# Optimization experiments

Measured on AMD Instinct MI355X. Metric: run time of the kernel, lower is better.

## Reference

```python
import jax, jax.numpy as jnp
import numpy as np

D_MODEL = 768
N_LAYER = 8
EXPAND = 2
D_INNER = EXPAND * D_MODEL          # 1536
HEADDIM = 64
NHEADS = D_INNER // HEADDIM         # 24
D_STATE = 128
D_CONV = 4
NGROUPS = 1
CONV_DIM = D_INNER + 2 * NGROUPS * D_STATE      # 1792
D_IN_PROJ = 2 * D_INNER + 2 * NGROUPS * D_STATE + NHEADS  # 3352
DIM_INP = 6
DIM_OUT = 5
BATCH = 4
SEQ = 2048
EPS = 1e-5


def rmsnorm(x, w):
    return x * jax.lax.rsqrt(jnp.mean(x * x, axis=-1, keepdims=True) + EPS) * w


def setup_inputs() -> dict:
    key = jax.random.key(0)
    ks = jax.random.split(key, 12)
    nrm = lambda k, shape, s=0.02: jax.random.normal(k, shape, jnp.float32) * s
    x = jax.random.normal(ks[0], (BATCH, SEQ, DIM_INP), jnp.float32)
    y = jax.random.normal(ks[1], (BATCH, SEQ, DIM_OUT), jnp.float32)
    W_emb = nrm(ks[2], (D_MODEL, DIM_INP))
    b_emb = jnp.zeros((D_MODEL,), jnp.float32)
    # stacked per-layer Mamba2 params
    W_in = nrm(ks[3], (N_LAYER, D_IN_PROJ, D_MODEL))
    conv_w = nrm(ks[4], (N_LAYER, CONV_DIM, D_CONV), 0.2)
    conv_b = jnp.zeros((N_LAYER, CONV_DIM), jnp.float32)
    dt0 = jax.random.uniform(ks[5], (N_LAYER, NHEADS), jnp.float32, 1e-3, 1e-1)
    dt_bias = jnp.log(jnp.expm1(dt0))  # inverse softplus of target dt
    A_log = jnp.log(jax.random.uniform(ks[6], (N_LAYER, NHEADS), jnp.float32, 1.0, 16.0))
    Dp = jnp.ones((N_LAYER, NHEADS), jnp.float32)
    norm_w = jnp.ones((N_LAYER, D_INNER), jnp.float32)     # gated RMSNorm inside Mamba2
    W_out = nrm(ks[7], (N_LAYER, D_MODEL, D_INNER))
    block_norm_w = jnp.ones((N_LAYER, D_MODEL), jnp.float32)  # prenorm RMSNorm per block
    norm_f_w = jnp.ones((D_MODEL,), jnp.float32)
    W_head = nrm(ks[8], (DIM_OUT, D_MODEL))
    return dict(x=x, y=y, W_emb=W_emb, b_emb=b_emb, W_in=W_in, conv_w=conv_w,
                conv_b=conv_b, dt_bias=dt_bias, A_log=A_log, Dp=Dp, norm_w=norm_w,
                W_out=W_out, block_norm_w=block_norm_w, norm_f_w=norm_f_w, W_head=W_head)


def _mamba2(u, W_in_l, conv_w_l, conv_b_l, dt_bias_l, A_log_l, D_l, norm_w_l, W_out_l):
    B, L, _ = u.shape
    zxbcdt = jnp.einsum('bld,ed->ble', u, W_in_l)  # [B,L,D_IN_PROJ]
    z = zxbcdt[..., :D_INNER]
    xBC = zxbcdt[..., D_INNER:D_INNER + CONV_DIM]
    dt = jax.nn.softplus(zxbcdt[..., D_INNER + CONV_DIM:] + dt_bias_l)  # [B,L,H]
    # causal depthwise conv1d, kernel D_CONV
    xp = jnp.pad(xBC, ((0, 0), (D_CONV - 1, 0), (0, 0)))
    xBC = sum(xp[:, k:k + L, :] * conv_w_l[:, k] for k in range(D_CONV)) + conv_b_l
    xBC = jax.nn.silu(xBC)
    xh = xBC[..., :D_INNER].reshape(B, L, NHEADS, HEADDIM)
    Bm = xBC[..., D_INNER:D_INNER + D_STATE]   # [B,L,N] (ngroups=1)
    Cm = xBC[..., D_INNER + D_STATE:]          # [B,L,N]
    A = -jnp.exp(A_log_l)                       # [H]
    decay = jnp.exp(dt * A)                     # [B,L,H]
    dtx = dt[..., None] * xh                    # [B,L,H,P]

    def step(h, inp):
        dec_t, dtx_t, B_t, C_t = inp            # [B,H],[B,H,P],[B,N],[B,N]
        h = h * dec_t[..., None, None] + dtx_t[..., None] * B_t[:, None, None, :]
        y_t = jnp.einsum('bhpn,bn->bhp', h, C_t)
        return h, y_t

    h0 = jnp.zeros((B, NHEADS, HEADDIM, D_STATE), u.dtype)
    _, ys = jax.lax.scan(step, h0, (decay.transpose(1, 0, 2), dtx.transpose(1, 0, 2, 3),
                                    Bm.transpose(1, 0, 2), Cm.transpose(1, 0, 2)))
    ys = ys.transpose(1, 0, 2, 3) + xh * D_l[None, None, :, None]  # skip term D*x
    yf = ys.reshape(B, L, D_INNER)
    yf = rmsnorm(yf * jax.nn.silu(z), norm_w_l)  # gated RMSNorm (norm_before_gate=False)
    return jnp.einsum('bld,ed->ble', yf, W_out_l)


def _forward(x, W_emb, b_emb, W_in, conv_w, conv_b, dt_bias, A_log, Dp, norm_w,
             W_out, block_norm_w, norm_f_w, W_head):
    h = jnp.einsum('bli,di->bld', x, W_emb) + b_emb
    res = jnp.zeros_like(h)

    def layer_step(carry, lp):
        h, res = carry
        Wi, cw, cb, dtb, Al, Dl, nw, Wo, bnw = lp
        res = h + res
        hn = rmsnorm(res, bnw)
        h = _mamba2(hn, Wi, cw, cb, dtb, Al, Dl, nw, Wo)
        return (h, res), None

    (h, res), _ = jax.lax.scan(layer_step, (h, res),
                               (W_in, conv_w, conv_b, dt_bias, A_log, Dp, norm_w, W_out, block_norm_w))
    res = h + res
    hn = rmsnorm(res, norm_f_w)
    return jnp.einsum('bld,od->blo', hn, W_head)


def reference(x, y, W_emb, b_emb, W_in, conv_w, conv_b, dt_bias, A_log, Dp, norm_w,
              W_out, block_norm_w, norm_f_w, W_head):
    out = _forward(x, W_emb, b_emb, W_in, conv_w, conv_b, dt_bias, A_log, Dp, norm_w,
                   W_out, block_norm_w, norm_f_w, W_head)
    loss = jnp.mean((out - y) ** 2)
    return out, loss
```

## Files before the change

### kernel.cpp

```cpp
#include <hip/hip_runtime.h>
#include <hip/hip_bf16.h>
#include <math.h>

#define BATCH 4
#define SEQ 2048
#define DMODEL 768
#define NLAYER 8
#define DINNER 1536
#define HEADDIM 64
#define NHEADS 24
#define DSTATE 128
#define CONVDIM 1792
#define DINPROJ 3352
#define NPAD 3456
#define ROWS (BATCH*SEQ)
#define EPS 1e-5f
#define QCH 128
#define NCH (SEQ/QCH)

typedef __bf16 bf16;
typedef bf16 bf16x8 __attribute__((ext_vector_type(8)));
typedef bf16 bf16x4 __attribute__((ext_vector_type(4)));
typedef float f32x4 __attribute__((ext_vector_type(4)));

#define GLD(src, dst) __builtin_amdgcn_global_load_lds( \
    (const __attribute__((address_space(1))) void*)(src), \
    (__attribute__((address_space(3))) void*)(dst), 16, 0, 0)

__device__ __forceinline__ void bar_sync() {
    asm volatile("" ::: "memory");
    __builtin_amdgcn_s_barrier();
    asm volatile("" ::: "memory");
}

__device__ __forceinline__ float fsilu(float x) { return x / (1.f + __expf(-x)); }

__global__ void k_embed(const float* __restrict__ x, const float* __restrict__ We,
                        const float* __restrict__ be, float* __restrict__ res) {
    int idx = blockIdx.x * 256 + threadIdx.x;
    int d = idx % DMODEL; int bl = idx / DMODEL;
    float acc = be[d];
#pragma unroll
    for (int i = 0; i < 6; ++i) acc += x[bl * 6 + i] * We[d * 6 + i];
    res[idx] = acc;
}

__global__ __launch_bounds__(256) void k_rmsnorm(const float* __restrict__ res,
                                                 const float* __restrict__ w,
                                                 bf16* __restrict__ out) {
    __shared__ float sm[4];
    int r = blockIdx.x, tid = threadIdx.x;
    float v[3]; float ss = 0.f;
#pragma unroll
    for (int k = 0; k < 3; ++k) {
        int d = tid + k * 256;
        float t = res[r * DMODEL + d];
        v[k] = t; ss += t * t;
    }
#pragma unroll
    for (int off = 32; off; off >>= 1) ss += __shfl_down(ss, off, 64);
    if ((tid & 63) == 0) sm[tid >> 6] = ss;
    __syncthreads();
    float tot = sm[0] + sm[1] + sm[2] + sm[3];
    float sc = rsqrtf(tot / (float)DMODEL + EPS);
#pragma unroll
    for (int k = 0; k < 3; ++k) {
        int d = tid + k * 256;
        out[r * DMODEL + d] = (bf16)(v[k] * sc * w[d]);
    }
}

__global__ void k_cvt_in(const float* __restrict__ src, bf16* __restrict__ dst) {
    int idx = blockIdx.x * 256 + threadIdx.x;
    int l = idx / (NPAD * DMODEL);
    int rem = idx % (NPAD * DMODEL);
    int n = rem / DMODEL;
    int d = rem % DMODEL;
    dst[idx] = (n < DINPROJ) ? (bf16)src[(long)l * DINPROJ * DMODEL + n * DMODEL + d] : (bf16)0.f;
}
__global__ void k_cvt_out(const float* __restrict__ src, bf16* __restrict__ dst) {
    int idx = blockIdx.x * 256 + threadIdx.x;
    dst[idx] = (bf16)src[idx];
}

template <typename OT, int BM, int BN, bool ACC>
__global__ __launch_bounds__(256) void k_gemm(const bf16* __restrict__ A, const bf16* __restrict__ B,
                                              OT* __restrict__ C, int K, int ldc) {
    constexpr int nWn = BN / 64;
    constexpr int nWm = 4 / nWn;
    constexpr int WMR = BM / nWm;
    constexpr int MI  = WMR / 16;
    constexpr int NI  = 4;
    constexpr int RG  = BM / 4;
    constexpr int BG  = BN / RG;
    __shared__ bf16 As[2][BM * 64];
    __shared__ bf16 Bs[2][BN * 64];
    const int tid = threadIdx.x;
    const int lane = tid & 63;
    const int w = tid >> 6;
    const int wm = w / nWn, wn = w % nWn;
    int wg = blockIdx.x + blockIdx.y * gridDim.x;
    int cpx = (gridDim.x * gridDim.y) >> 3;
    int swz = (wg & 7) * cpx + (wg >> 3);
    int bx = swz % gridDim.x;
    int by = swz / gridDim.x;
    const long rowA0 = (long)bx * BM;
    const long rowB0 = (long)by * BN;
    const int srow = tid >> 3;
    const int scol = ((tid & 7) ^ (srow & 7)) * 8;
    const bf16* Ab = A + rowA0 * K + scol;
    const bf16* Bb = B + rowB0 * K + scol;

    f32x4 acc[MI][NI];
    const f32x4 vz = {0.f, 0.f, 0.f, 0.f};
#pragma unroll
    for (int mi = 0; mi < MI; ++mi)
#pragma unroll
        for (int ni = 0; ni < NI; ++ni) acc[mi][ni] = vz;

    auto stage = [&](int buf, int kt) {
#pragma unroll
        for (int j = 0; j < 4; ++j)
            GLD(Ab + (long)(j * RG + srow) * K + kt, &As[buf][(j * RG + w * 8) * 64]);
#pragma unroll
        for (int j = 0; j < BG; ++j)
            GLD(Bb + (long)(j * RG + srow) * K + kt, &Bs[buf][(j * RG + w * 8) * 64]);
    };
    auto waitv = [&]() {
        if constexpr (BG == 4) asm volatile("s_waitcnt vmcnt(8)" ::: "memory");
        else                   asm volatile("s_waitcnt vmcnt(6)" ::: "memory");
    };
    auto compute = [&](int buf) {
        const char* AsB = (const char*)As[buf];
        const char* BsB = (const char*)Bs[buf];
#pragma unroll
        for (int s = 0; s < 2; ++s) {
            bf16x8 af[MI], bfr[NI];
#pragma unroll
            for (int mi = 0; mi < MI; ++mi) {
                int r = wm * WMR + mi * 16 + (lane & 15);
                af[mi] = *(const bf16x8*)(AsB + r * 128 + ((s * 64 + (lane >> 4) * 16) ^ ((r & 7) << 4)));
            }
#pragma unroll
            for (int ni = 0; ni < NI; ++ni) {
                int r = wn * 64 + ni * 16 + (lane & 15);
                bfr[ni] = *(const bf16x8*)(BsB + r * 128 + ((s * 64 + (lane >> 4) * 16) ^ ((r & 7) << 4)));
            }
#pragma unroll
            for (int mi = 0; mi < MI; ++mi)
#pragma unroll
                for (int ni = 0; ni < NI; ++ni)
                    acc[mi][ni] = __builtin_amdgcn_mfma_f32_16x16x32_bf16(af[mi], bfr[ni], acc[mi][ni], 0, 0, 0);
        }
    };

    stage(0, 0);
    stage(1, 64);
    int cur = 0;
    for (int kt = 128; kt < K; kt += 64) {
        waitv();
        bar_sync();
        compute(cur);
        bar_sync();
        stage(cur, kt);
        cur ^= 1;
    }
    waitv();
    bar_sync();
    compute(cur);
    asm volatile("s_waitcnt vmcnt(0)" ::: "memory");
    bar_sync();
    compute(cur ^ 1);

    const int crow = (lane >> 4) * 4;
    const int ccol = lane & 15;
#pragma unroll
    for (int mi = 0; mi < MI; ++mi)
#pragma unroll
        for (int ni = 0; ni < NI; ++ni) {
            long r0 = rowA0 + wm * WMR + mi * 16 + crow;
            long c0 = rowB0 + wn * 64 + ni * 16 + ccol;
#pragma unroll
            for (int j = 0; j < 4; ++j) {
                if constexpr (ACC) C[(r0 + j) * ldc + c0] += (OT)acc[mi][ni][j];
                else               C[(r0 + j) * ldc + c0]  = (OT)acc[mi][ni][j];
            }
        }
}

__global__ void k_convBC(const bf16* __restrict__ zx, const float* __restrict__ cw,
                         const float* __restrict__ cb, bf16* __restrict__ bc) {
    int idx = blockIdx.x * 256 + threadIdx.x;
    int c8 = idx & 31; int blt = idx >> 5;
    int t = blt % SEQ;
    int ch = DINNER + c8 * 8;
    long bbase = (long)(blt - t) * NPAD;
    float cwa[8][4];
#pragma unroll
    for (int j = 0; j < 8; ++j) {
        float4 tv = *(const float4*)(cw + (ch + j) * 4);
        cwa[j][0] = tv.x; cwa[j][1] = tv.y; cwa[j][2] = tv.z; cwa[j][3] = tv.w;
    }
    float acc[8];
#pragma unroll
    for (int j = 0; j < 8; ++j) acc[j] = cb[ch + j];
#pragma unroll
    for (int k = 0; k < 4; ++k) {
        int tt = t + k - 3;
        if (tt >= 0) {
            bf16x8 v = *(const bf16x8*)(zx + bbase + (long)tt * NPAD + DINNER + ch);
#pragma unroll
            for (int j = 0; j < 8; ++j) acc[j] += (float)v[j] * cwa[j][k];
        }
    }
    bf16x8 o;
#pragma unroll
    for (int j = 0; j < 8; ++j) o[j] = (bf16)fsilu(acc[j]);
    *(bf16x8*)(bc + (long)blt * 256 + c8 * 8) = o;
}

__global__ __launch_bounds__(256) void k_prepL(const bf16* __restrict__ zx, const bf16* __restrict__ bc,
                                               const float* __restrict__ cw_l, const float* __restrict__ cb_l,
                                               const float* __restrict__ dt_bias_l,
                                               const float* __restrict__ Alog,
                                               float* __restrict__ Sarr, float* __restrict__ dtc,
                                               float* __restrict__ Pcb,
                                               bf16* __restrict__ XT, bf16* __restrict__ Lbuf) {
    __shared__ float S_lds[128], wl_lds[128], wtot[2];
    __shared__ bf16 Xs[136 * 64];
    __shared__ bf16 Xw[64 * 128];
    __shared__ bf16 Bt[128 * 128];
    int blk = blockIdx.x;
    int b = blk / (NHEADS * NCH);
    int r = blk % (NHEADS * NCH);
    int h = r / NCH;
    int c = r % NCH;
    int tid = threadIdx.x, lane = tid & 63, wid = tid >> 6;
    long brow0 = (long)b * SEQ + c * QCH;
#pragma unroll
    for (int i = 0; i < 5; ++i) {
        int base = i * 256 + wid * 64;
        if (base < 1048) {
            int idx = base + lane;
            long g = brow0 - 3 + (idx >> 3);
            if (g < 0) g = 0;
            if (g > (long)ROWS - 1) g = (long)ROWS - 1;
            GLD(zx + g * NPAD + DINNER + h * HEADDIM + (idx & 7) * 8,
                (char*)Xs + (long)base * 16);
        }
    }
    float ps = 0.f, dtv = 0.f;
    if (tid < 128) {
        float raw = (float)zx[(brow0 + tid) * NPAD + DINNER + CONVDIM + h] + dt_bias_l[h];
        dtv = (raw > 15.f) ? raw : log1pf(__expf(raw));
        float Ah = -__expf(Alog[h]);
        ps = dtv * Ah;
#pragma unroll
        for (int off = 1; off < 64; off <<= 1) {
            float o = __shfl_up(ps, off, 64);
            if ((tid & 63) >= off) ps += o;
        }
        if ((tid & 63) == 63) wtot[tid >> 6] = ps;
    }
    __syncthreads();
    if (tid < 128) {
        if (tid >= 64) ps += wtot[0];
        S_lds[tid] = ps;
    }
    __syncthreads();
    float Sl = S_lds[127];
    if (tid < 128) {
        wl_lds[tid] = __expf(Sl - ps) * dtv;
        Sarr[blk * QCH + tid] = ps;
        dtc[blk * QCH + tid] = dtv;
        if (tid == 127) Pcb[blk] = __expf(Sl);
    }
    __syncthreads();
    {
        int p = tid >> 2, q = tid & 3;
        float4 cwv = *(const float4*)(cw_l + (h * HEADDIM + p) * 4);
        float cbv = cb_l[h * HEADDIM + p];
        float cwa[4] = {cwv.x, cwv.y, cwv.z, cwv.w};
        char* xtb = (char*)XT + (((long)blk) << 14);
#pragma unroll
        for (int ub = 0; ub < 4; ++ub) {
            int u0 = q * 32 + ub * 8;
            bf16x8 vx, vw;
#pragma unroll
            for (int k = 0; k < 8; ++k) {
                int u = u0 + k;
                float a = cbv;
#pragma unroll
                for (int tt = 0; tt < 4; ++tt) {
                    if (c > 0 || u + tt >= 3)
                        a += (float)Xs[(u + tt) * 64 + p] * cwa[tt];
                }
                bf16 xb = (bf16)fsilu(a);
                vx[k] = xb;
                vw[k] = (bf16)((float)xb * wl_lds[u]);
            }
            long off = (long)((p * 256 + u0 * 2) ^ ((p & 7) << 4));
            *(bf16x8*)(xtb + off) = vx;
            *(bf16x8*)((char*)Xw + off) = vw;
        }
    }
#pragma unroll
    for (int nb = 0; nb < 2; ++nb) {
        __syncthreads();
#pragma unroll
        for (int i = 0; i < 4; ++i) {
            int idx = i * 256 + tid;
            GLD(bc + (brow0 + (idx >> 3)) * 256 + nb * 64 + (idx & 7) * 8,
                (char*)Xs + (i * 256 + wid * 64) * 16);
        }
        __syncthreads();
        int nl = tid >> 2, q = tid & 3;
        int n = nb * 64 + nl;
#pragma unroll
        for (int ub = 0; ub < 4; ++ub) {
            int u0 = q * 32 + ub * 8;
            bf16x8 v;
#pragma unroll
            for (int k = 0; k < 8; ++k) v[k] = Xs[(u0 + k) * 64 + nl];
            long off = (long)((n * 256 + u0 * 2) ^ ((n & 7) << 4));
            *(bf16x8*)((char*)Bt + off) = v;
        }
    }
    __syncthreads();
    f32x4 acc[4][2];
    const f32x4 vz = {0.f, 0.f, 0.f, 0.f};
#pragma unroll
    for (int mi = 0; mi < 4; ++mi)
#pragma unroll
        for (int ni = 0; ni < 2; ++ni) acc[mi][ni] = vz;
    const char* XwB = (const char*)Xw;
    const char* BtB = (const char*)Bt;
    __builtin_amdgcn_s_setprio(1);
#pragma unroll
    for (int ks = 0; ks < 4; ++ks) {
        bf16x8 af[4], bfr[2];
#pragma unroll
        for (int mi = 0; mi < 4; ++mi) {
            int pp = mi * 16 + (lane & 15);
            af[mi] = *(const bf16x8*)(XwB + ((pp * 256 + ks * 64 + (lane >> 4) * 16) ^ ((pp & 7) << 4)));
        }
#pragma unroll
        for (int ni = 0; ni < 2; ++ni) {
            int n = wid * 32 + ni * 16 + (lane & 15);
            bfr[ni] = *(const bf16x8*)(BtB + ((n * 256 + ks * 64 + (lane >> 4) * 16) ^ ((n & 7) << 4)));
        }
#pragma unroll
        for (int mi = 0; mi < 4; ++mi)
#pragma unroll
            for (int ni = 0; ni < 2; ++ni)
                acc[mi][ni] = __builtin_amdgcn_mfma_f32_16x16x32_bf16(af[mi], bfr[ni], acc[mi][ni], 0, 0, 0);
    }
    __builtin_amdgcn_s_setprio(0);
    char* lb = (char*)Lbuf + (((long)blk) << 14);
#pragma unroll
    for (int mi = 0; mi < 4; ++mi)
#pragma unroll
        for (int ni = 0; ni < 2; ++ni)
#pragma unroll
            for (int j = 0; j < 4; ++j) {
                int pp = mi * 16 + (lane >> 4) * 4 + j;
                int n = wid * 32 + ni * 16 + (lane & 15);
                *(bf16*)(lb + ((pp * 256 + n * 2) ^ ((pp & 7) << 4))) = (bf16)acc[mi][ni][j];
            }
}

__global__ __launch_bounds__(256) void k_scanB(bf16* __restrict__ Lbuf, const float* __restrict__ Pc) {
    int bh = blockIdx.x >> 2;
    int q = blockIdx.x & 3;
    int off = (q * 256 + threadIdx.x) * 8;
    long base = ((long)bh * NCH) << 13;
    float s[8] = {0.f};
#pragma unroll
    for (int c = 0; c < NCH; ++c) {
        bf16* p = Lbuf + base + ((long)c << 13) + off;
        bf16x8 L = *(bf16x8*)p;
        bf16x8 I;
#pragma unroll
        for (int k = 0; k < 8; ++k) I[k] = (bf16)s[k];
        float P = Pc[bh * NCH + c];
#pragma unroll
        for (int k = 0; k < 8; ++k) s[k] = P * s[k] + (float)L[k];
        *(bf16x8*)p = I;
    }
}

__global__ __launch_bounds__(512) void k_chunkY(const bf16* __restrict__ bc,
                                                const float* __restrict__ Sarr, const float* __restrict__ dtc,
                                                const float* __restrict__ Dp,
                                                const bf16* __restrict__ XT, const bf16* __restrict__ Lbuf,
                                                bf16* __restrict__ ysb) {
    __shared__ bf16 Cs[128 * 128];
    __shared__ bf16 Bs[128 * 128];
    __shared__ bf16 Xts[64 * 128];
    __shared__ bf16 Is[64 * 128];
    __shared__ float S_lds[128], dt_lds[128];
    int blk = blockIdx.x;
    int b = blk / (NHEADS * NCH);
    int r = blk % (NHEADS * NCH);
    int h = r / NCH;
    int c = r % NCH;
    int tid = threadIdx.x, lane = tid & 63, wid = tid >> 6;
    long brow0 = (long)b * SEQ + c * QCH;
    const char* bcB = (const char*)bc;
#pragma unroll
    for (int i = 0; i < 4; ++i) {
        int trow = i * 32 + wid * 4 + (lane >> 4);
        int blk16 = lane & 15;
        const char* rp = bcB + (brow0 + trow) * 512;
        int sb = (blk16 ^ (trow & 7)) << 4;
        GLD(rp + 256 + sb, (char*)Cs + (i * 32 + wid * 4) * 256);
        GLD(rp + sb,       (char*)Bs + (i * 32 + wid * 4) * 256);
    }
    const char* xt = (const char*)XT + (((long)blk) << 14);
    const char* ib = (const char*)Lbuf + (((long)blk) << 14);
#pragma unroll
    for (int i = 0; i < 2; ++i) {
        GLD(xt + (long)(i * 512 + tid) * 16, (char*)Xts + (i * 512 + wid * 64) * 16);
        GLD(ib + (long)(i * 512 + tid) * 16, (char*)Is + (i * 512 + wid * 64) * 16);
    }
    if (tid < 128) { S_lds[tid] = Sarr[blk * QCH + tid]; dt_lds[tid] = dtc[blk * QCH + tid]; }
    float Dh = Dp[h];
    asm volatile("s_waitcnt vmcnt(4) lgkmcnt(0)" ::: "memory");
    bar_sync();
    const char* CsB = (const char*)Cs;
    char* BsB = (char*)Bs;
    const char* IsB = (const char*)Is;
    const char* XtB = (const char*)Xts;
    const f32x4 vz = {0.f, 0.f, 0.f, 0.f};
    int wmG = wid >> 2, wnG = wid & 3;
    f32x4 accg[4][2];
#pragma unroll
    for (int mi = 0; mi < 4; ++mi)
#pragma unroll
        for (int ni = 0; ni < 2; ++ni) accg[mi][ni] = vz;
#pragma unroll
    for (int ks = 0; ks < 4; ++ks) {
        bf16x8 af[4], bfr[2];
#pragma unroll
        for (int mi = 0; mi < 4; ++mi) {
            int t = wmG * 64 + mi * 16 + (lane & 15);
            af[mi] = *(const bf16x8*)(CsB + ((t * 256 + ks * 64 + (lane >> 4) * 16) ^ ((t & 7) << 4)));
        }
#pragma unroll
        for (int ni = 0; ni < 2; ++ni) {
            int u = wnG * 32 + ni * 16 + (lane & 15);
            bfr[ni] = *(const bf16x8*)(BsB + ((u * 256 + ks * 64 + (lane >> 4) * 16) ^ ((u & 7) << 4)));
        }
#pragma unroll
        for (int mi = 0; mi < 4; ++mi)
#pragma unroll
            for (int ni = 0; ni < 2; ++ni)
                accg[mi][ni] = __builtin_amdgcn_mfma_f32_16x16x32_bf16(af[mi], bfr[ni], accg[mi][ni], 0, 0, 0);
    }
    bar_sync();
#pragma unroll
    for (int mi = 0; mi < 4; ++mi) {
#pragma unroll
        for (int j = 0; j < 4; ++j) {
            int t = wmG * 64 + mi * 16 + (lane >> 4) * 4 + j;
            float St = S_lds[t];
#pragma unroll
            for (int ni = 0; ni < 2; ++ni) {
                int u = wnG * 32 + ni * 16 + (lane & 15);
                float v = 0.f;
                if (u <= t) v = accg[mi][ni][j] * __expf(St - S_lds[u]) * dt_lds[u];
                *(bf16*)(BsB + ((t * 256 + u * 2) ^ ((t & 7) << 4))) = (bf16)v;
            }
        }
    }
    asm volatile("s_waitcnt vmcnt(0) lgkmcnt(0)" ::: "memory");
    bar_sync();
    int wmY = wid >> 1, wnY = wid & 1;
    f32x4 accy[2][2];
#pragma unroll
    for (int mi = 0; mi < 2; ++mi)
#pragma unroll
        for (int ni = 0; ni < 2; ++ni) accy[mi][ni] = vz;
#pragma unroll
    for (int ks = 0; ks < 4; ++ks) {
        bf16x8 af[2], bfr[2];
#pragma unroll
        for (int mi = 0; mi < 2; ++mi) {
            int t = wmY * 32 + mi * 16 + (lane & 15);
            af[mi] = *(const bf16x8*)(CsB + ((t * 256 + ks * 64 + (lane >> 4) * 16) ^ ((t & 7) << 4)));
        }
#pragma unroll
        for (int ni = 0; ni < 2; ++ni) {
            int pp = wnY * 32 + ni * 16 + (lane & 15);
            bfr[ni] = *(const bf16x8*)(IsB + ((pp * 256 + ks * 64 + (lane >> 4) * 16) ^ ((pp & 7) << 4)));
        }
#pragma unroll
        for (int mi = 0; mi < 2; ++mi)
#pragma unroll
            for (int ni = 0; ni < 2; ++ni)
                accy[mi][ni] = __builtin_amdgcn_mfma_f32_16x16x32_bf16(af[mi], bfr[ni], accy[mi][ni], 0, 0, 0);
    }
#pragma unroll
    for (int mi = 0; mi < 2; ++mi)
#pragma unroll
        for (int j = 0; j < 4; ++j) {
            int t = wmY * 32 + mi * 16 + (lane >> 4) * 4 + j;
            float e = __expf(S_lds[t]);
#pragma unroll
            for (int ni = 0; ni < 2; ++ni) accy[mi][ni][j] *= e;
        }
#pragma unroll
    for (int ks = 0; ks < 4; ++ks) {
        bf16x8 af[2], bfr[2];
#pragma unroll
        for (int mi = 0; mi < 2; ++mi) {
            int t = wmY * 32 + mi * 16 + (lane & 15);
            af[mi] = *(const bf16x8*)(BsB + ((t * 256 + ks * 64 + (lane >> 4) * 16) ^ ((t & 7) << 4)));
        }
#pragma unroll
        for (int ni = 0; ni < 2; ++ni) {
            int pp = wnY * 32 + ni * 16 + (lane & 15);
            bfr[ni] = *(const bf16x8*)(XtB + ((pp * 256 + ks * 64 + (lane >> 4) * 16) ^ ((pp & 7) << 4)));
        }
#pragma unroll
        for (int mi = 0; mi < 2; ++mi)
#pragma unroll
            for (int ni = 0; ni < 2; ++ni)
                accy[mi][ni] = __builtin_amdgcn_mfma_f32_16x16x32_bf16(af[mi], bfr[ni], accy[mi][ni], 0, 0, 0);
    }
#pragma unroll
    for (int mi = 0; mi < 2; ++mi)
#pragma unroll
        for (int ni = 0; ni < 2; ++ni)
#pragma unroll
            for (int j = 0; j < 4; ++j) {
                int t = wmY * 32 + mi * 16 + (lane >> 4) * 4 + j;
                int pp = wnY * 32 + ni * 16 + (lane & 15);
                float xv = (float)*(const bf16*)(XtB + ((pp * 256 + t * 2) ^ ((pp & 7) << 4)));
                ysb[(brow0 + t) * DINNER + h * HEADDIM + pp] = (bf16)(accy[mi][ni][j] + Dh * xv);
            }
}

__global__ __launch_bounds__(256) void k_gated(const bf16* __restrict__ ys, const bf16* __restrict__ zx,
                                               const float* __restrict__ w, bf16* __restrict__ out) {
    __shared__ float sm[4];
    int r = blockIdx.x, tid = threadIdx.x;
    float v[6]; float ss = 0.f;
#pragma unroll
    for (int k = 0; k < 6; ++k) {
        int d = tid + k * 256;
        float z = (float)zx[(long)r * NPAD + d];
        float t = (float)ys[(long)r * DINNER + d] * fsilu(z);
        v[k] = t; ss += t * t;
    }
#pragma unroll
    for (int off = 32; off; off >>= 1) ss += __shfl_down(ss, off, 64);
    if ((tid & 63) == 0) sm[tid >> 6] = ss;
    __syncthreads();
    float tot = sm[0] + sm[1] + sm[2] + sm[3];
    float sc = rsqrtf(tot / (float)DINNER + EPS);
#pragma unroll
    for (int k = 0; k < 6; ++k) {
        int d = tid + k * 256;
        out[(long)r * DINNER + d] = (bf16)(v[k] * sc * w[d]);
    }
}

__global__ __launch_bounds__(256) void k_head(const bf16* __restrict__ hn, const float* __restrict__ Wh,
                                              const float* __restrict__ y, float* __restrict__ out,
                                              float* __restrict__ loss) {
    __shared__ float sl[4];
    int tid = threadIdx.x, lane = tid & 63, wid = tid >> 6;
    float wv[5][12];
#pragma unroll
    for (int o = 0; o < 5; ++o)
#pragma unroll
        for (int j = 0; j < 12; ++j) wv[o][j] = Wh[o * DMODEL + lane * 12 + j];
    float lsum = 0.f;
#pragma unroll
    for (int rr = 0; rr < 8; ++rr) {
        long r = (long)blockIdx.x * 32 + wid * 8 + rr;
        const bf16* hp = hn + r * DMODEL + lane * 12;
        float hv[12];
#pragma unroll
        for (int q = 0; q < 3; ++q) {
            bf16x4 v4 = *(const bf16x4*)(hp + q * 4);
#pragma unroll
            for (int j = 0; j < 4; ++j) hv[q * 4 + j] = (float)v4[j];
        }
        float acc[5];
#pragma unroll
        for (int o = 0; o < 5; ++o) {
            float a = 0.f;
#pragma unroll
            for (int j = 0; j < 12; ++j) a += hv[j] * wv[o][j];
            acc[o] = a;
        }
#pragma unroll
        for (int o = 0; o < 5; ++o)
#pragma unroll
            for (int m = 32; m; m >>= 1) acc[o] += __shfl_xor(acc[o], m, 64);
        if (lane == 0) {
#pragma unroll
            for (int o = 0; o < 5; ++o) {
                out[r * 5 + o] = acc[o];
                float d = acc[o] - y[r * 5 + o];
                lsum += d * d;
            }
        }
    }
    if (lane == 0) sl[wid] = lsum;
    __syncthreads();
    if (tid == 0) atomicAdd(loss, (sl[0] + sl[1] + sl[2] + sl[3]) * (1.f / ((float)ROWS * 5.f)));
}

extern "C" void kernel_launch(void* const* d_in, const int* in_sizes, int n_in,
                              void* d_out, int out_size, void* d_ws, size_t ws_size,
                              hipStream_t stream) {
    const float* x      = (const float*)d_in[0];
    const float* y      = (const float*)d_in[1];
    const float* W_emb  = (const float*)d_in[2];
    const float* b_emb  = (const float*)d_in[3];
    const float* W_in   = (const float*)d_in[4];
    const float* conv_w = (const float*)d_in[5];
    const float* conv_b = (const float*)d_in[6];
    const float* dt_bias= (const float*)d_in[7];
    const float* A_log  = (const float*)d_in[8];
    const float* Dp     = (const float*)d_in[9];
    const float* norm_w = (const float*)d_in[10];
    const float* W_out  = (const float*)d_in[11];
    const float* bnw    = (const float*)d_in[12];
    const float* nfw    = (const float*)d_in[13];
    const float* W_head = (const float*)d_in[14];

    char* ws = (char*)d_ws;
    float* res  = (float*)ws;  ws += (size_t)ROWS * DMODEL * 4;
    bf16*  Lbuf = (bf16*)ws;   ws += (size_t)BATCH * NHEADS * NCH * 8192 * 2;
    bf16*  hnb  = (bf16*)ws;   ws += (size_t)ROWS * DMODEL * 2;
    bf16*  zx   = (bf16*)ws;   ws += (size_t)ROWS * NPAD * 2;
    bf16*  bc   = (bf16*)ws;   ws += (size_t)ROWS * 256 * 2;
    bf16*  ysb  = (bf16*)ws;   ws += (size_t)ROWS * DINNER * 2;
    bf16*  yfb  = (bf16*)ws;   ws += (size_t)ROWS * DINNER * 2;
    bf16*  Wib  = (bf16*)ws;   ws += (size_t)NLAYER * NPAD * DMODEL * 2;
    bf16*  Wob  = (bf16*)ws;   ws += (size_t)NLAYER * DMODEL * DINNER * 2;
    float* Pcb  = (float*)ws;  ws += (size_t)BATCH * NHEADS * NCH * 4;
    float* Sarr = (float*)ws;  ws += (size_t)BATCH * NHEADS * NCH * QCH * 4;
    float* dtc  = (float*)ws;  ws += (size_t)BATCH * NHEADS * NCH * QCH * 4;
    bf16*  XT   = (bf16*)ws;   ws += (size_t)BATCH * NHEADS * NCH * 8192 * 2;

    float* out_p  = (float*)d_out;
    float* loss_p = out_p + (size_t)ROWS * 5;

    hipMemsetAsync(loss_p, 0, 4, stream);
    k_embed<<<ROWS * DMODEL / 256, 256, 0, stream>>>(x, W_emb, b_emb, res);
    k_cvt_in<<<NLAYER * NPAD * DMODEL / 256, 256, 0, stream>>>(W_in, Wib);
    k_cvt_out<<<NLAYER * DMODEL * DINNER / 256, 256, 0, stream>>>(W_out, Wob);

    const int NBHC = BATCH * NHEADS * NCH;
    for (int l = 0; l < NLAYER; ++l) {
        const float* cw_l = conv_w + (size_t)l * CONVDIM * 4;
        const float* cb_l = conv_b + (size_t)l * CONVDIM;
        k_rmsnorm<<<ROWS, 256, 0, stream>>>(res, bnw + l * DMODEL, hnb);
        dim3 g1(ROWS / 128, NPAD / 128);
        k_gemm<bf16, 128, 128, false><<<g1, 256, 0, stream>>>(hnb, Wib + (size_t)l * NPAD * DMODEL, zx, DMODEL, NPAD);
        k_convBC<<<ROWS * 32 / 256, 256, 0, stream>>>(zx, cw_l, cb_l, bc);
        k_prepL<<<NBHC, 256, 0, stream>>>(zx, bc, cw_l, cb_l, dt_bias + l * NHEADS, A_log + l * NHEADS,
                                          Sarr, dtc, Pcb, XT, Lbuf);
        k_scanB<<<BATCH * NHEADS * 4, 256, 0, stream>>>(Lbuf, Pcb);
        k_chunkY<<<NBHC, 512, 0, stream>>>(bc, Sarr, dtc, Dp + l * NHEADS, XT, Lbuf, ysb);
        k_gated<<<ROWS, 256, 0, stream>>>(ysb, zx, norm_w + l * DINNER, yfb);
        dim3 g2(ROWS / 128, DMODEL / 64);
        k_gemm<float, 128, 64, true><<<g2, 256, 0, stream>>>(yfb, Wob + (size_t)l * DMODEL * DINNER, res, DINNER, DMODEL);
    }

    k_rmsnorm<<<ROWS, 256, 0, stream>>>(res, nfw, hnb);
    k_head<<<256, 256, 0, stream>>>(hnb, W_head, y, out_p, loss_p);
}
```

Before: 1.979 ms.

## Use 256x256 tiles with 512 threads for the input-projection GEMM

Generalizes the GEMM template over thread count and switches the in-projection GEMM to 256x256 tiles run by 512-thread workgroups. The weight buffer is padded to 3584 columns, and a column bound check stops writes past the real 3456-wide output. It also drops the blockIdx swizzle for L2 locality. Larger tiles improve operand reuse and cut redundant loads, but they reduce the workgroup count (32x14 = 448), raise LDS use to 128KB per block, and may lower occupancy.

```diff
diff --git a/kernel.cpp b/kernel.cpp
--- a/kernel.cpp
+++ b/kernel.cpp
@@ -13,6 +13,7 @@
 #define CONVDIM 1792
 #define DINPROJ 3352
 #define NPAD 3456
+#define NPADW 3584
 #define ROWS (BATCH*SEQ)
 #define EPS 1e-5f
 #define QCH 128
@@ -72,8 +73,8 @@
 
 __global__ void k_cvt_in(const float* __restrict__ src, bf16* __restrict__ dst) {
     int idx = blockIdx.x * 256 + threadIdx.x;
-    int l = idx / (NPAD * DMODEL);
-    int rem = idx % (NPAD * DMODEL);
+    int l = idx / (NPADW * DMODEL);
+    int rem = idx % (NPADW * DMODEL);
     int n = rem / DMODEL;
     int d = rem % DMODEL;
     dst[idx] = (n < DINPROJ) ? (bf16)src[(long)l * DINPROJ * DMODEL + n * DMODEL + d] : (bf16)0.f;
@@ -83,15 +84,17 @@
     dst[idx] = (bf16)src[idx];
 }
 
-template <typename OT, int BM, int BN, bool ACC>
-__global__ __launch_bounds__(256) void k_gemm(const bf16* __restrict__ A, const bf16* __restrict__ B,
-                                              OT* __restrict__ C, int K, int ldc) {
-    constexpr int nWn = BN / 64;
-    constexpr int nWm = 4 / nWn;
+template <typename OT, int BM, int BN, int TH, bool ACC>
+__global__ __launch_bounds__(TH) void k_gemm(const bf16* __restrict__ A, const bf16* __restrict__ B,
+                                             OT* __restrict__ C, int K, int ldc, int Nact) {
+    constexpr int NW  = TH / 64;
+    constexpr int nWn = (BN / 64 < 4) ? BN / 64 : 4;
+    constexpr int nWm = NW / nWn;
     constexpr int WMR = BM / nWm;
     constexpr int MI  = WMR / 16;
     constexpr int NI  = 4;
-    constexpr int RG  = BM / 4;
+    constexpr int RG  = TH / 8;
+    constexpr int AG  = BM / RG;
     constexpr int BG  = BN / RG;
     __shared__ bf16 As[2][BM * 64];
     __shared__ bf16 Bs[2][BN * 64];
@@ -99,13 +102,8 @@
     const int lane = tid & 63;
     const int w = tid >> 6;
     const int wm = w / nWn, wn = w % nWn;
-    int wg = blockIdx.x + blockIdx.y * gridDim.x;
-    int cpx = (gridDim.x * gridDim.y) >> 3;
-    int swz = (wg & 7) * cpx + (wg >> 3);
-    int bx = swz % gridDim.x;
-    int by = swz / gridDim.x;
-    const long rowA0 = (long)bx * BM;
-    const long rowB0 = (long)by * BN;
+    const long rowA0 = (long)blockIdx.x * BM;
+    const long rowB0 = (long)blockIdx.y * BN;
     const int srow = tid >> 3;
     const int scol = ((tid & 7) ^ (srow & 7)) * 8;
     const bf16* Ab = A + rowA0 * K + scol;
@@ -120,15 +118,15 @@
 
     auto stage = [&](int buf, int kt) {
 #pragma unroll
-        for (int j = 0; j < 4; ++j)
-            GLD(Ab + (long)(j * RG + srow) * K + kt, &As[buf][(j * RG + w * 8) * 64]);
+        for (int j = 0; j < AG; ++j)
+            GLD(Ab + (long)(j * RG + srow) * K + kt, &As[buf][(j * TH + w * 64) * 8]);
 #pragma unroll
         for (int j = 0; j < BG; ++j)
-            GLD(Bb + (long)(j * RG + srow) * K + kt, &Bs[buf][(j * RG + w * 8) * 64]);
+            GLD(Bb + (long)(j * RG + srow) * K + kt, &Bs[buf][(j * TH + w * 64) * 8]);
     };
     auto waitv = [&]() {
-        if constexpr (BG == 4) asm volatile("s_waitcnt vmcnt(8)" ::: "memory");
-        else                   asm volatile("s_waitcnt vmcnt(6)" ::: "memory");
+        if constexpr (AG + BG == 8) asm volatile("s_waitcnt vmcnt(8)" ::: "memory");
+        else                        asm volatile("s_waitcnt vmcnt(6)" ::: "memory");
     };
     auto compute = [&](int buf) {
         const char* AsB = (const char*)As[buf];
@@ -180,10 +178,12 @@
         for (int ni = 0; ni < NI; ++ni) {
             long r0 = rowA0 + wm * WMR + mi * 16 + crow;
             long c0 = rowB0 + wn * 64 + ni * 16 + ccol;
-#pragma unroll
-            for (int j = 0; j < 4; ++j) {
-                if constexpr (ACC) C[(r0 + j) * ldc + c0] += (OT)acc[mi][ni][j];
-                else               C[(r0 + j) * ldc + c0]  = (OT)acc[mi][ni][j];
+            if ((int)c0 < Nact) {
+#pragma unroll
+                for (int j = 0; j < 4; ++j) {
+                    if constexpr (ACC) C[(r0 + j) * ldc + c0] += (OT)acc[mi][ni][j];
+                    else               C[(r0 + j) * ldc + c0]  = (OT)acc[mi][ni][j];
+                }
             }
         }
 }
@@ -641,7 +641,7 @@
     bf16*  bc   = (bf16*)ws;   ws += (size_t)ROWS * 256 * 2;
     bf16*  ysb  = (bf16*)ws;   ws += (size_t)ROWS * DINNER * 2;
     bf16*  yfb  = (bf16*)ws;   ws += (size_t)ROWS * DINNER * 2;
-    bf16*  Wib  = (bf16*)ws;   ws += (size_t)NLAYER * NPAD * DMODEL * 2;
+    bf16*  Wib  = (bf16*)ws;   ws += (size_t)NLAYER * NPADW * DMODEL * 2;
     bf16*  Wob  = (bf16*)ws;   ws += (size_t)NLAYER * DMODEL * DINNER * 2;
     float* Pcb  = (float*)ws;  ws += (size_t)BATCH * NHEADS * NCH * 4;
     float* Sarr = (float*)ws;  ws += (size_t)BATCH * NHEADS * NCH * QCH * 4;
@@ -653,7 +653,7 @@
 
     hipMemsetAsync(loss_p, 0, 4, stream);
     k_embed<<<ROWS * DMODEL / 256, 256, 0, stream>>>(x, W_emb, b_emb, res);
-    k_cvt_in<<<NLAYER * NPAD * DMODEL / 256, 256, 0, stream>>>(W_in, Wib);
+    k_cvt_in<<<NLAYER * NPADW * DMODEL / 256, 256, 0, stream>>>(W_in, Wib);
     k_cvt_out<<<NLAYER * DMODEL * DINNER / 256, 256, 0, stream>>>(W_out, Wob);
 
     const int NBHC = BATCH * NHEADS * NCH;
@@ -661,8 +661,8 @@
         const float* cw_l = conv_w + (size_t)l * CONVDIM * 4;
         const float* cb_l = conv_b + (size_t)l * CONVDIM;
         k_rmsnorm<<<ROWS, 256, 0, stream>>>(res, bnw + l * DMODEL, hnb);
-        dim3 g1(ROWS / 128, NPAD / 128);
-        k_gemm<bf16, 128, 128, false><<<g1, 256, 0, stream>>>(hnb, Wib + (size_t)l * NPAD * DMODEL, zx, DMODEL, NPAD);
+        dim3 g1(ROWS / 256, NPADW / 256);
+        k_gemm<bf16, 256, 256, 512, false><<<g1, 512, 0, stream>>>(hnb, Wib + (size_t)l * NPADW * DMODEL, zx, DMODEL, NPAD, NPAD);
         k_convBC<<<ROWS * 32 / 256, 256, 0, stream>>>(zx, cw_l, cb_l, bc);
         k_prepL<<<NBHC, 256, 0, stream>>>(zx, bc, cw_l, cb_l, dt_bias + l * NHEADS, A_log + l * NHEADS,
                                           Sarr, dtc, Pcb, XT, Lbuf);
@@ -670,7 +670,7 @@
         k_chunkY<<<NBHC, 512, 0, stream>>>(bc, Sarr, dtc, Dp + l * NHEADS, XT, Lbuf, ysb);
         k_gated<<<ROWS, 256, 0, stream>>>(ysb, zx, norm_w + l * DINNER, yfb);
         dim3 g2(ROWS / 128, DMODEL / 64);
-        k_gemm<float, 128, 64, true><<<g2, 256, 0, stream>>>(yfb, Wob + (size_t)l * DMODEL * DINNER, res, DINNER, DMODEL);
+        k_gemm<float, 128, 64, 256, true><<<g2, 256, 0, stream>>>(yfb, Wob + (size_t)l * DMODEL * DINNER, res, DINNER, DMODEL, DMODEL);
     }
 
     k_rmsnorm<<<ROWS, 256, 0, stream>>>(res, nfw, hnb);
```

After: 1.741 ms. -12.0%, faster.
